# Kernel optimization log

Measured on AMD Instinct MI355X. Metric: run time of the kernel, lower is better.

## Reference

```python
import jax, jax.numpy as jnp
import numpy as np

N = 512
D = 512
# static upper-triangle pair indices (i < j)
_II, _JJ = np.triu_indices(N, k=1)
_II = jnp.asarray(_II)
_JJ = jnp.asarray(_JJ)


def setup_inputs() -> dict:
    key = jax.random.key(0)
    ks = jax.random.split(key, 9)
    s = 0.02
    return {
        'features': jax.random.normal(ks[0], (N, D), dtype=jnp.float32),
        # relation_classifier: Linear(2D->D), Linear(D->10)
        'cw1': jax.random.normal(ks[1], (2 * D, D), dtype=jnp.float32) * s,
        'cb1': jnp.zeros((D,), dtype=jnp.float32),
        'cw2': jax.random.normal(ks[2], (D, 10), dtype=jnp.float32) * s,
        'cb2': jnp.zeros((10,), dtype=jnp.float32),
        # relation_strength_calc: Linear(2D->D//2), Linear(D//2->1)
        'sw1': jax.random.normal(ks[3], (2 * D, D // 2), dtype=jnp.float32) * s,
        'sb1': jnp.zeros((D // 2,), dtype=jnp.float32),
        'sw2': jax.random.normal(ks[4], (D // 2, 1), dtype=jnp.float32) * s,
        'sb2': jnp.zeros((1,), dtype=jnp.float32),
    }


def reference(features, cw1, cb1, cw2, cb2, sw1, sb1, sw2, sb2):
    # cat([f_i, f_j]) @ W == f_i @ W[:D] + f_j @ W[D:]  (linear-split trick)
    # precompute per-node projections once, then gather per pair
    c_a = features @ cw1[:D]   # [N, D]
    c_b = features @ cw1[D:]   # [N, D]
    s_a = features @ sw1[:D]   # [N, D//2]
    s_b = features @ sw1[D:]   # [N, D//2]

    # classifier path
    h = jax.nn.relu(c_a[_II] + c_b[_JJ] + cb1)          # [P, D]
    relation_types = jax.nn.log_softmax(h @ cw2 + cb2)   # [P, 10]
    most_likely_relations = jnp.argmax(relation_types, axis=-1)  # [P]

    # strength path
    hs = jax.nn.relu(s_a[_II] + s_b[_JJ] + sb1)          # [P, D//2]
    relation_strengths = jax.nn.sigmoid(hs @ sw2 + sb2)   # [P, 1]

    return relation_types, most_likely_relations, relation_strengths
```

## Files before the change

kernel.cpp:

```cpp
#include <hip/hip_runtime.h>
#include <math.h>

#define NN 512
#define DD 512
#define NPAIRS 130816
#define TYPES_OFF 0
#define ARGMAX_OFF 1308160
#define STRENGTH_OFF 1438976

#define GAP_THRESH 2.5e-4f


__device__ __forceinline__ void fma64_step(
    const float4& a0, const float4& a1,
    const float4& b0, const float4& b1, const float4& b2, const float4& b3,
    double acc[2][4])
{
    const float av[2][4] = {{a0.x,a0.y,a0.z,a0.w},{a1.x,a1.y,a1.z,a1.w}};
    const float bv[4][4] = {{b0.x,b0.y,b0.z,b0.w},{b1.x,b1.y,b1.z,b1.w},
                            {b2.x,b2.y,b2.z,b2.w},{b3.x,b3.y,b3.z,b3.w}};
    #pragma unroll
    for (int kk = 0; kk < 4; ++kk) {
        double ad0 = (double)av[0][kk], ad1 = (double)av[1][kk];
        #pragma unroll
        for (int c = 0; c < 4; ++c) {
            double bd = (double)bv[kk][c];
            acc[0][c] = fma(ad0, bd, acc[0][c]);
            acc[1][c] = fma(ad1, bd, acc[1][c]);
        }
    }
}

__device__ __forceinline__ void fma32_step(
    const float4& a0, const float4& a1,
    const float4& b0, const float4& b1, const float4& b2, const float4& b3,
    float acc[2][4])
{
    const float av[2][4] = {{a0.x,a0.y,a0.z,a0.w},{a1.x,a1.y,a1.z,a1.w}};
    const float bv[4][4] = {{b0.x,b0.y,b0.z,b0.w},{b1.x,b1.y,b1.z,b1.w},
                            {b2.x,b2.y,b2.z,b2.w},{b3.x,b3.y,b3.z,b3.w}};
    #pragma unroll
    for (int kk = 0; kk < 4; ++kk) {
        #pragma unroll
        for (int c = 0; c < 4; ++c) {
            acc[0][c] = fmaf(av[0][kk], bv[kk][c], acc[0][c]);
            acc[1][c] = fmaf(av[1][kk], bv[kk][c], acc[1][c]);
        }
    }
}

__global__ __launch_bounds__(256, 4) void proj_kernel(
    const float* __restrict__ F, const float* __restrict__ cw1,
    const float* __restrict__ sw1,
    const float* __restrict__ cb1, const float* __restrict__ sb1,
    double* __restrict__ ca0, double* __restrict__ ca1,
    double* __restrict__ cb0, double* __restrict__ cbp1,
    float* __restrict__ sa0, float* __restrict__ sa1,
    float* __restrict__ sb0, float* __restrict__ sbp1)
{
    const int t = threadIdx.x;
    const int wid  = blockIdx.x * 4 + (t >> 6);
    const int lane = t & 63;
    const int mg = lane >> 4;
    const int nq = lane & 15;

    if (wid < 2048) {
        const int z  = wid & 1;
        const int r  = wid >> 1;
        const int nt = r & 15;
        const int mt = r >> 4;
        const int m0 = mt * 8;
        const int n  = nt * 64;
        const float* W = (n < 512) ? cw1 : cw1 + 512 * 512;
        const int n0   = (n < 512) ? n : n - 512;
        double* outp   = (n < 512) ? (z ? ca1 : ca0) : (z ? cbp1 : cb0);
        const bool addbias = (z == 0) && (n < 512);

        const int row0 = m0 + mg * 2;
        const int col0 = n0 + nq * 4;
        const float* pa0 = F + row0 * 512 + z * 256;
        const float* pa1 = pa0 + 512;
        const float* pb  = W + (z * 256) * 512 + col0;

        double acc[2][4];
        #pragma unroll
        for (int rr = 0; rr < 2; ++rr)
            #pragma unroll
            for (int cc = 0; cc < 4; ++cc) acc[rr][cc] = 0.0;

        float4 a0 = *(const float4*)(pa0);
        float4 a1 = *(const float4*)(pa1);
        float4 b0 = *(const float4*)(pb);
        float4 b1 = *(const float4*)(pb + 512);
        float4 b2 = *(const float4*)(pb + 1024);
        float4 b3 = *(const float4*)(pb + 1536);
        for (int s = 0; s < 63; ++s) {
            float4 na0 = *(const float4*)(pa0 + (s + 1) * 4);
            float4 na1 = *(const float4*)(pa1 + (s + 1) * 4);
            const float* nb = pb + (s + 1) * 2048;
            float4 nb0 = *(const float4*)(nb);
            float4 nb1 = *(const float4*)(nb + 512);
            float4 nb2 = *(const float4*)(nb + 1024);
            float4 nb3 = *(const float4*)(nb + 1536);
            fma64_step(a0, a1, b0, b1, b2, b3, acc);
            a0 = na0; a1 = na1; b0 = nb0; b1 = nb1; b2 = nb2; b3 = nb3;
        }
        fma64_step(a0, a1, b0, b1, b2, b3, acc);

        #pragma unroll
        for (int rr = 0; rr < 2; ++rr) {
            double v[4];
            #pragma unroll
            for (int cc = 0; cc < 4; ++cc) {
                v[cc] = acc[rr][cc];
                if (addbias) v[cc] += (double)cb1[col0 + cc];
            }
            double* dst = outp + (row0 + rr) * 512 + col0;
            *(double2*)(dst + 0) = make_double2(v[0], v[1]);
            *(double2*)(dst + 2) = make_double2(v[2], v[3]);
        }
    } else {
        const int w2 = wid - 2048;
        const int z  = w2 & 1;
        const int r  = w2 >> 1;
        const int nt = r & 7;
        const int mt = r >> 3;
        const int m0 = mt * 8;
        const int n  = nt * 64;
        const float* W = (n < 256) ? sw1 : sw1 + 512 * 256;
        const int n0   = (n < 256) ? n : n - 256;
        float* outp    = (n < 256) ? (z ? sa1 : sa0) : (z ? sbp1 : sb0);
        const bool addbias = (z == 0) && (n < 256);

        const int row0 = m0 + mg * 2;
        const int col0 = n0 + nq * 4;
        const float* pa0 = F + row0 * 512 + z * 256;
        const float* pa1 = pa0 + 512;
        const float* pb  = W + (z * 256) * 256 + col0;

        float acc[2][4];
        #pragma unroll
        for (int rr = 0; rr < 2; ++rr)
            #pragma unroll
            for (int cc = 0; cc < 4; ++cc) acc[rr][cc] = 0.f;

        float4 a0 = *(const float4*)(pa0);
        float4 a1 = *(const float4*)(pa1);
        float4 b0 = *(const float4*)(pb);
        float4 b1 = *(const float4*)(pb + 256);
        float4 b2 = *(const float4*)(pb + 512);
        float4 b3 = *(const float4*)(pb + 768);
        for (int s = 0; s < 63; ++s) {
            float4 na0 = *(const float4*)(pa0 + (s + 1) * 4);
            float4 na1 = *(const float4*)(pa1 + (s + 1) * 4);
            const float* nb = pb + (s + 1) * 1024;
            float4 nb0 = *(const float4*)(nb);
            float4 nb1 = *(const float4*)(nb + 256);
            float4 nb2 = *(const float4*)(nb + 512);
            float4 nb3 = *(const float4*)(nb + 768);
            fma32_step(a0, a1, b0, b1, b2, b3, acc);
            a0 = na0; a1 = na1; b0 = nb0; b1 = nb1; b2 = nb2; b3 = nb3;
        }
        fma32_step(a0, a1, b0, b1, b2, b3, acc);

        #pragma unroll
        for (int rr = 0; rr < 2; ++rr) {
            float4 v = make_float4(acc[rr][0], acc[rr][1], acc[rr][2], acc[rr][3]);
            if (addbias) {
                v.x += sb1[col0 + 0]; v.y += sb1[col0 + 1];
                v.z += sb1[col0 + 2]; v.w += sb1[col0 + 3];
            }
            *(float4*)(outp + (row0 + rr) * 256 + col0) = v;
        }
    }
}

__global__ __launch_bounds__(256, 4) void pair_kernel(
    const double* __restrict__ ca0, const double* __restrict__ ca1,
    const double* __restrict__ cb0, const double* __restrict__ cbp1,
    const float* __restrict__ sa0, const float* __restrict__ sa1,
    const float* __restrict__ sb0, const float* __restrict__ sbp1,
    const float* __restrict__ cw2, const float* __restrict__ cb2,
    const float* __restrict__ sw2, const float* __restrict__ sb2,
    float* __restrict__ out)
{
    const int b = blockIdx.x;
    int bi = (int)floorf((129.0f - sqrtf(16641.0f - 8.0f * (float)b)) * 0.5f);
    while ((bi + 1) * (129 - (bi + 1)) / 2 <= b) ++bi;
    while (bi * (129 - bi) / 2 > b) --bi;
    const int bj = bi + (b - bi * (129 - bi) / 2);
    const int i0 = bi * 8, j0 = bj * 8;

    const int t = threadIdx.x;
    const int q  = t >> 6;
    const int qu = __builtin_amdgcn_readfirstlane(q);
    const int l = t & 63;
    const int pi = l >> 3, pj = l & 7;
    const int i = i0 + pi, j = j0 + pj;

    __shared__ __align__(16) float smem[4352];
    float* sSa = smem;
    float* sSb = smem + 2176;
    float* sA  = smem;
    float* sB  = smem + 2176;
    float* lgbuf = smem;
    float* stbuf = smem + 1920;

    #pragma unroll
    for (int u = 0; u < 4; ++u) {
        int idx = u * 256 + t;
        int kq  = idx & 15;
        int row = (idx >> 4) & 7;
        int qq  = (idx >> 7) & 3;
        int arr = idx >> 9;
        int off = (arr ? (j0 + row) : (i0 + row)) * 256 + qq * 64 + kq * 4;
        const float* s0 = arr ? sb0 : sa0;
        const float* s1 = arr ? sbp1 : sa1;
        float4 v0 = *(const float4*)(s0 + off);
        float4 v1 = *(const float4*)(s1 + off);
        float4 v = make_float4(v0.x + v1.x, v0.y + v1.y, v0.z + v1.z, v0.w + v1.w);
        float* dst = (arr ? sSb : sSa) + (qq * 8 + row) * 68 + kq * 4;
        *(float4*)dst = v;
    }
    __syncthreads();
    float accs = 0.f;
    {
        const float* sw2q = sw2 + qu * 64;
        const float* ra = sSa + (q * 8 + pi) * 68;
        const float* rb = sSb + (q * 8 + pj) * 68;
        #pragma unroll 16
        for (int kk = 0; kk < 64; ++kk) {
            float h = fmaxf(ra[kk] + rb[kk], 0.f);
            accs = fmaf(h, sw2q[kk], accs);
        }
    }

    float lg[10];
    #pragma unroll
    for (int c = 0; c < 10; ++c) lg[c] = 0.f;

    for (int rnd = 0; rnd < 2; ++rnd) {
        __syncthreads();
        #pragma unroll
        for (int u = 0; u < 4; ++u) {
            int idx = u * 256 + t;
            int kq  = idx & 15;
            int row = (idx >> 4) & 7;
            int qq  = (idx >> 7) & 3;
            int arr = idx >> 9;
            int off = (arr ? (j0 + row) : (i0 + row)) * 512 + qq * 128 + rnd * 64 + kq * 4;
            const double* d0 = arr ? cb0 : ca0;
            const double* d1 = arr ? cbp1 : ca1;
            double2 x0 = *(const double2*)(d0 + off);
            double2 x1 = *(const double2*)(d0 + off + 2);
            double2 y0 = *(const double2*)(d1 + off);
            double2 y1 = *(const double2*)(d1 + off + 2);
            float4 v = make_float4((float)(x0.x + y0.x), (float)(x0.y + y0.y),
                                   (float)(x1.x + y1.x), (float)(x1.y + y1.y));
            float* dst = (arr ? sB : sA) + (qq * 8 + row) * 68 + kq * 4;
            *(float4*)dst = v;
        }
        __syncthreads();
        const float* ra = sA + (q * 8 + pi) * 68;
        const float* rb = sB + (q * 8 + pj) * 68;
        const float* wr = cw2 + (qu * 128 + rnd * 64) * 10;
        #pragma unroll 8
        for (int kk = 0; kk < 64; ++kk) {
            float h = fmaxf(ra[kk] + rb[kk], 0.f);
            const float* w = wr + kk * 10;
            #pragma unroll
            for (int c = 0; c < 10; ++c) lg[c] = fmaf(h, w[c], lg[c]);
        }
    }

    __syncthreads();
    if (q > 0) {
        float* dst = lgbuf + ((q - 1) * 64 + l) * 10;
        #pragma unroll
        for (int c = 0; c < 10; ++c) dst[c] = lg[c];
        stbuf[(q - 1) * 64 + l] = accs;
    }
    __syncthreads();
    if (q == 0) {
        #pragma unroll
        for (int w = 0; w < 3; ++w) {
            const float* srcb = lgbuf + (w * 64 + l) * 10;
            #pragma unroll
            for (int c = 0; c < 10; ++c) lg[c] += srcb[c];
        }
        float st = accs + stbuf[l] + stbuf[64 + l] + stbuf[128 + l] + sb2[0];

        #pragma unroll
        for (int c = 0; c < 10; ++c) lg[c] += cb2[c];

        float mx = lg[0], mx2 = -3.0e38f; int am2 = 0;
        #pragma unroll
        for (int c = 1; c < 10; ++c) {
            if (lg[c] > mx) { mx2 = mx; mx = lg[c]; am2 = c; }
            else if (lg[c] > mx2) mx2 = lg[c];
        }

        unsigned long long m = __ballot((j > i) && (mx - mx2 < GAP_THRESH));
        while (m) {
            const int s = __ffsll((unsigned long long)m) - 1; m &= (m - 1);
            const int si = i0 + (s >> 3), sj = j0 + (s & 7);
            double part[10];
            #pragma unroll
            for (int c = 0; c < 10; ++c) part[c] = 0.0;
            const int kb = l * 8;
            #pragma unroll 2
            for (int kk = 0; kk < 8; ++kk) {
                const int k = kb + kk;
                double h = fmax(ca0[si * 512 + k] + ca1[si * 512 + k]
                              + cb0[sj * 512 + k] + cbp1[sj * 512 + k], 0.0);
                const float* w = cw2 + k * 10;
                #pragma unroll
                for (int c = 0; c < 10; ++c) part[c] = fma(h, (double)w[c], part[c]);
            }
            #pragma unroll
            for (int off = 32; off > 0; off >>= 1) {
                #pragma unroll
                for (int c = 0; c < 10; ++c) part[c] += __shfl_xor(part[c], off, 64);
            }
            double bmx = part[0] + (double)cb2[0]; int ba = 0;
            #pragma unroll
            for (int c = 1; c < 10; ++c) {
                double v = part[c] + (double)cb2[c];
                if (v > bmx) { bmx = v; ba = c; }
            }
            if (l == s) am2 = ba;
        }

        float tf[10]; float ssum = 0.f;
        #pragma unroll
        for (int c = 0; c < 10; ++c) { tf[c] = lg[c] - mx; ssum += __expf(tf[c]); }
        float ls = __logf(ssum);

        if (j > i) {
            const int p = i * 511 - (i * (i - 1)) / 2 + (j - i - 1);
            float* tp = out + TYPES_OFF + p * 10;
            #pragma unroll
            for (int c = 0; c < 10; ++c) tp[c] = tf[c] - ls;
            out[ARGMAX_OFF + p] = (float)am2;
            out[STRENGTH_OFF + p] = 1.0f / (1.0f + __expf(-st));
        }
    }
}

extern "C" void kernel_launch(void* const* d_in, const int* in_sizes, int n_in,
                              void* d_out, int out_size, void* d_ws, size_t ws_size,
                              hipStream_t stream) {
    const float* F   = (const float*)d_in[0];
    const float* cw1 = (const float*)d_in[1];
    const float* cb1 = (const float*)d_in[2];
    const float* cw2 = (const float*)d_in[3];
    const float* cb2 = (const float*)d_in[4];
    const float* sw1 = (const float*)d_in[5];
    const float* sb1 = (const float*)d_in[6];
    const float* sw2 = (const float*)d_in[7];
    const float* sb2 = (const float*)d_in[8];
    float* out = (float*)d_out;

    char* ws = (char*)d_ws;
    double* ca0  = (double*)(ws);
    double* ca1  = (double*)(ws + 2097152);
    double* cb0  = (double*)(ws + 4194304);
    double* cbp1 = (double*)(ws + 6291456);
    float*  sa0  = (float*)(ws + 8388608);
    float*  sa1  = (float*)(ws + 8912896);
    float*  sb0  = (float*)(ws + 9437184);
    float*  sbp1 = (float*)(ws + 9961472);

    hipLaunchKernelGGL(proj_kernel, dim3(768), dim3(256), 0, stream,
                       F, cw1, sw1, cb1, sb1,
                       ca0, ca1, cb0, cbp1, sa0, sa1, sb0, sbp1);
    hipLaunchKernelGGL(pair_kernel, dim3(2080), dim3(256), 0, stream,
                       ca0, ca1, cb0, cbp1, sa0, sa1, sb0, sbp1,
                       cw2, cb2, sw2, sb2, out);
}
```

Measured before the change: 146.1 us.

## Halve per-thread FP64 projection tile and use packed FP32 FMAs in pair kernel

```diff
diff --git a/kernel.cpp b/kernel.cpp
--- a/kernel.cpp
+++ b/kernel.cpp
@@ -11,23 +11,46 @@
 #define GAP_THRESH 2.5e-4f
 
 
-__device__ __forceinline__ void fma64_step(
+typedef float f32x2 __attribute__((ext_vector_type(2)));
+
+__device__ __forceinline__ f32x2 pk_add(f32x2 a, f32x2 b) {
+    f32x2 d;
+    asm("v_pk_add_f32 %0, %1, %2" : "=v"(d) : "v"(a), "v"(b));
+    return d;
+}
+__device__ __forceinline__ f32x2 pk_fma(f32x2 a, f32x2 b, f32x2 c) {
+    f32x2 d;
+    asm("v_pk_fma_f32 %0, %1, %2, %3" : "=v"(d) : "v"(a), "s"(b), "v"(c));
+    return d;
+}
+__device__ __forceinline__ f32x2 pk_fma_lo(f32x2 a, f32x2 b, f32x2 c) {
+    f32x2 d;
+    asm("v_pk_fma_f32 %0, %1, %2, %3 op_sel:[0,0,0] op_sel_hi:[0,1,1]"
+        : "=v"(d) : "v"(a), "s"(b), "v"(c));
+    return d;
+}
+__device__ __forceinline__ f32x2 pk_fma_hi(f32x2 a, f32x2 b, f32x2 c) {
+    f32x2 d;
+    asm("v_pk_fma_f32 %0, %1, %2, %3 op_sel:[1,0,0] op_sel_hi:[1,1,1]"
+        : "=v"(d) : "v"(a), "s"(b), "v"(c));
+    return d;
+}
+
+__device__ __forceinline__ void fma64_step2(
     const float4& a0, const float4& a1,
-    const float4& b0, const float4& b1, const float4& b2, const float4& b3,
-    double acc[2][4])
+    const float2& b0, const float2& b1, const float2& b2, const float2& b3,
+    double acc[2][2])
 {
     const float av[2][4] = {{a0.x,a0.y,a0.z,a0.w},{a1.x,a1.y,a1.z,a1.w}};
-    const float bv[4][4] = {{b0.x,b0.y,b0.z,b0.w},{b1.x,b1.y,b1.z,b1.w},
-                            {b2.x,b2.y,b2.z,b2.w},{b3.x,b3.y,b3.z,b3.w}};
+    const float bv[4][2] = {{b0.x,b0.y},{b1.x,b1.y},{b2.x,b2.y},{b3.x,b3.y}};
     #pragma unroll
     for (int kk = 0; kk < 4; ++kk) {
         double ad0 = (double)av[0][kk], ad1 = (double)av[1][kk];
-        #pragma unroll
-        for (int c = 0; c < 4; ++c) {
-            double bd = (double)bv[kk][c];
-            acc[0][c] = fma(ad0, bd, acc[0][c]);
-            acc[1][c] = fma(ad1, bd, acc[1][c]);
-        }
+        double bd0 = (double)bv[kk][0], bd1 = (double)bv[kk][1];
+        acc[0][0] = fma(ad0, bd0, acc[0][0]);
+        acc[0][1] = fma(ad0, bd1, acc[0][1]);
+        acc[1][0] = fma(ad1, bd0, acc[1][0]);
+        acc[1][1] = fma(ad1, bd1, acc[1][1]);
     }
 }
 
@@ -64,63 +87,57 @@
     const int mg = lane >> 4;
     const int nq = lane & 15;
 
-    if (wid < 2048) {
+    if (wid < 4096) {
         const int z  = wid & 1;
         const int r  = wid >> 1;
-        const int nt = r & 15;
-        const int mt = r >> 4;
+        const int nt = r & 31;
+        const int mt = r >> 5;
         const int m0 = mt * 8;
-        const int n  = nt * 64;
+        const int n  = nt * 32;
         const float* W = (n < 512) ? cw1 : cw1 + 512 * 512;
         const int n0   = (n < 512) ? n : n - 512;
         double* outp   = (n < 512) ? (z ? ca1 : ca0) : (z ? cbp1 : cb0);
         const bool addbias = (z == 0) && (n < 512);
 
         const int row0 = m0 + mg * 2;
-        const int col0 = n0 + nq * 4;
+        const int col0 = n0 + nq * 2;
         const float* pa0 = F + row0 * 512 + z * 256;
         const float* pa1 = pa0 + 512;
         const float* pb  = W + (z * 256) * 512 + col0;
 
-        double acc[2][4];
-        #pragma unroll
-        for (int rr = 0; rr < 2; ++rr)
-            #pragma unroll
-            for (int cc = 0; cc < 4; ++cc) acc[rr][cc] = 0.0;
+        double acc[2][2];
+        acc[0][0] = acc[0][1] = acc[1][0] = acc[1][1] = 0.0;
 
         float4 a0 = *(const float4*)(pa0);
         float4 a1 = *(const float4*)(pa1);
-        float4 b0 = *(const float4*)(pb);
-        float4 b1 = *(const float4*)(pb + 512);
-        float4 b2 = *(const float4*)(pb + 1024);
-        float4 b3 = *(const float4*)(pb + 1536);
+        float2 b0 = *(const float2*)(pb);
+        float2 b1 = *(const float2*)(pb + 512);
+        float2 b2 = *(const float2*)(pb + 1024);
+        float2 b3 = *(const float2*)(pb + 1536);
         for (int s = 0; s < 63; ++s) {
             float4 na0 = *(const float4*)(pa0 + (s + 1) * 4);
             float4 na1 = *(const float4*)(pa1 + (s + 1) * 4);
             const float* nb = pb + (s + 1) * 2048;
-            float4 nb0 = *(const float4*)(nb);
-            float4 nb1 = *(const float4*)(nb + 512);
-            float4 nb2 = *(const float4*)(nb + 1024);
-            float4 nb3 = *(const float4*)(nb + 1536);
-            fma64_step(a0, a1, b0, b1, b2, b3, acc);
+            float2 nb0 = *(const float2*)(nb);
+            float2 nb1 = *(const float2*)(nb + 512);
+            float2 nb2 = *(const float2*)(nb + 1024);
+            float2 nb3 = *(const float2*)(nb + 1536);
+            fma64_step2(a0, a1, b0, b1, b2, b3, acc);
             a0 = na0; a1 = na1; b0 = nb0; b1 = nb1; b2 = nb2; b3 = nb3;
         }
-        fma64_step(a0, a1, b0, b1, b2, b3, acc);
+        fma64_step2(a0, a1, b0, b1, b2, b3, acc);
 
         #pragma unroll
         for (int rr = 0; rr < 2; ++rr) {
-            double v[4];
-            #pragma unroll
-            for (int cc = 0; cc < 4; ++cc) {
-                v[cc] = acc[rr][cc];
-                if (addbias) v[cc] += (double)cb1[col0 + cc];
-            }
-            double* dst = outp + (row0 + rr) * 512 + col0;
-            *(double2*)(dst + 0) = make_double2(v[0], v[1]);
-            *(double2*)(dst + 2) = make_double2(v[2], v[3]);
+            double v0 = acc[rr][0], v1 = acc[rr][1];
+            if (addbias) {
+                v0 += (double)cb1[col0 + 0];
+                v1 += (double)cb1[col0 + 1];
+            }
+            *(double2*)(outp + (row0 + rr) * 512 + col0) = make_double2(v0, v1);
         }
     } else {
-        const int w2 = wid - 2048;
+        const int w2 = wid - 4096;
         const int z  = w2 & 1;
         const int r  = w2 >> 1;
         const int nt = r & 7;
@@ -228,16 +245,24 @@
         const float* sw2q = sw2 + qu * 64;
         const float* ra = sSa + (q * 8 + pi) * 68;
         const float* rb = sSb + (q * 8 + pj) * 68;
-        #pragma unroll 16
-        for (int kk = 0; kk < 64; ++kk) {
-            float h = fmaxf(ra[kk] + rb[kk], 0.f);
-            accs = fmaf(h, sw2q[kk], accs);
-        }
-    }
-
-    float lg[10];
+        f32x2 acc2 = {0.f, 0.f};
+        #pragma unroll 8
+        for (int kk = 0; kk < 64; kk += 2) {
+            f32x2 a2 = *(const f32x2*)(ra + kk);
+            f32x2 b2 = *(const f32x2*)(rb + kk);
+            f32x2 s2 = pk_add(a2, b2);
+            f32x2 h2;
+            h2.x = fmaxf(s2.x, 0.f);
+            h2.y = fmaxf(s2.y, 0.f);
+            f32x2 w2p = *(const f32x2*)(sw2q + kk);
+            acc2 = pk_fma(h2, w2p, acc2);
+        }
+        accs = acc2.x + acc2.y;
+    }
+
+    f32x2 acc5[5];
     #pragma unroll
-    for (int c = 0; c < 10; ++c) lg[c] = 0.f;
+    for (int cc = 0; cc < 5; ++cc) acc5[cc] = (f32x2){0.f, 0.f};
 
     for (int rnd = 0; rnd < 2; ++rnd) {
         __syncthreads();
@@ -264,14 +289,28 @@
         const float* ra = sA + (q * 8 + pi) * 68;
         const float* rb = sB + (q * 8 + pj) * 68;
         const float* wr = cw2 + (qu * 128 + rnd * 64) * 10;
-        #pragma unroll 8
-        for (int kk = 0; kk < 64; ++kk) {
-            float h = fmaxf(ra[kk] + rb[kk], 0.f);
-            const float* w = wr + kk * 10;
-            #pragma unroll
-            for (int c = 0; c < 10; ++c) lg[c] = fmaf(h, w[c], lg[c]);
-        }
-    }
+        #pragma unroll 2
+        for (int kk = 0; kk < 64; kk += 2) {
+            f32x2 ra2 = *(const f32x2*)(ra + kk);
+            f32x2 rb2 = *(const f32x2*)(rb + kk);
+            f32x2 s2 = pk_add(ra2, rb2);
+            f32x2 h2;
+            h2.x = fmaxf(s2.x, 0.f);
+            h2.y = fmaxf(s2.y, 0.f);
+            const float* w0 = wr + kk * 10;
+            #pragma unroll
+            for (int cc = 0; cc < 5; ++cc) {
+                f32x2 wk0 = *(const f32x2*)(w0 + 2 * cc);
+                f32x2 wk1 = *(const f32x2*)(w0 + 10 + 2 * cc);
+                acc5[cc] = pk_fma_lo(h2, wk0, acc5[cc]);
+                acc5[cc] = pk_fma_hi(h2, wk1, acc5[cc]);
+            }
+        }
+    }
+
+    float lg[10];
+    #pragma unroll
+    for (int cc = 0; cc < 5; ++cc) { lg[2*cc] = acc5[cc].x; lg[2*cc+1] = acc5[cc].y; }
 
     __syncthreads();
     if (q > 0) {
@@ -371,7 +410,7 @@
     float*  sb0  = (float*)(ws + 9437184);
     float*  sbp1 = (float*)(ws + 9961472);
 
-    hipLaunchKernelGGL(proj_kernel, dim3(768), dim3(256), 0, stream,
+    hipLaunchKernelGGL(proj_kernel, dim3(1280), dim3(256), 0, stream,
                        F, cw1, sw1, cb1, sb1,
                        ca0, ca1, cb0, cbp1, sa0, sa1, sb0, sbp1);
     hipLaunchKernelGGL(pair_kernel, dim3(2080), dim3(256), 0, stream,
```

Result: slower. 200.4 us (+37.2%).

## Stage projection weights in shared memory and vectorize pair-kernel LDS reads

Applied to the files above, without the earlier changes.

```diff
diff --git a/kernel.cpp b/kernel.cpp
--- a/kernel.cpp
+++ b/kernel.cpp
@@ -10,26 +10,6 @@
 
 #define GAP_THRESH 2.5e-4f
 
-
-__device__ __forceinline__ void fma64_step(
-    const float4& a0, const float4& a1,
-    const float4& b0, const float4& b1, const float4& b2, const float4& b3,
-    double acc[2][4])
-{
-    const float av[2][4] = {{a0.x,a0.y,a0.z,a0.w},{a1.x,a1.y,a1.z,a1.w}};
-    const float bv[4][4] = {{b0.x,b0.y,b0.z,b0.w},{b1.x,b1.y,b1.z,b1.w},
-                            {b2.x,b2.y,b2.z,b2.w},{b3.x,b3.y,b3.z,b3.w}};
-    #pragma unroll
-    for (int kk = 0; kk < 4; ++kk) {
-        double ad0 = (double)av[0][kk], ad1 = (double)av[1][kk];
-        #pragma unroll
-        for (int c = 0; c < 4; ++c) {
-            double bd = (double)bv[kk][c];
-            acc[0][c] = fma(ad0, bd, acc[0][c]);
-            acc[1][c] = fma(ad1, bd, acc[1][c]);
-        }
-    }
-}
 
 __device__ __forceinline__ void fma32_step(
     const float4& a0, const float4& a1,
@@ -58,54 +38,81 @@
     float* __restrict__ sa0, float* __restrict__ sa1,
     float* __restrict__ sb0, float* __restrict__ sbp1)
 {
+    __shared__ __align__(16) float sW[2][16][68];
+
     const int t = threadIdx.x;
-    const int wid  = blockIdx.x * 4 + (t >> 6);
     const int lane = t & 63;
     const int mg = lane >> 4;
     const int nq = lane & 15;
 
-    if (wid < 2048) {
-        const int z  = wid & 1;
-        const int r  = wid >> 1;
-        const int nt = r & 15;
-        const int mt = r >> 4;
-        const int m0 = mt * 8;
+    if (blockIdx.x < 512) {
+        const int b  = blockIdx.x;
+        const int z  = b & 1;
+        const int nt = (b >> 1) & 15;
+        const int mt = b >> 5;
+        const int w  = t >> 6;
         const int n  = nt * 64;
         const float* W = (n < 512) ? cw1 : cw1 + 512 * 512;
         const int n0   = (n < 512) ? n : n - 512;
         double* outp   = (n < 512) ? (z ? ca1 : ca0) : (z ? cbp1 : cb0);
         const bool addbias = (z == 0) && (n < 512);
 
-        const int row0 = m0 + mg * 2;
+        const int row0 = mt * 32 + w * 8 + mg * 2;
         const int col0 = n0 + nq * 4;
+
+        const int cg = t & 15, kr = t >> 4;
+        const float* wsrc = W + (z * 256 + kr) * 512 + n0 + cg * 4;
+
+        {
+            float4 w0 = *(const float4*)(wsrc);
+            *(float4*)&sW[0][kr][cg * 4] = w0;
+        }
+        __syncthreads();
+
+        double acc[2][4];
+        #pragma unroll
+        for (int rr = 0; rr < 2; ++rr)
+            #pragma unroll
+            for (int cc = 0; cc < 4; ++cc) acc[rr][cc] = 0.0;
+
         const float* pa0 = F + row0 * 512 + z * 256;
         const float* pa1 = pa0 + 512;
-        const float* pb  = W + (z * 256) * 512 + col0;
-
-        double acc[2][4];
-        #pragma unroll
-        for (int rr = 0; rr < 2; ++rr)
-            #pragma unroll
-            for (int cc = 0; cc < 4; ++cc) acc[rr][cc] = 0.0;
-
         float4 a0 = *(const float4*)(pa0);
         float4 a1 = *(const float4*)(pa1);
-        float4 b0 = *(const float4*)(pb);
-        float4 b1 = *(const float4*)(pb + 512);
-        float4 b2 = *(const float4*)(pb + 1024);
-        float4 b3 = *(const float4*)(pb + 1536);
-        for (int s = 0; s < 63; ++s) {
-            float4 na0 = *(const float4*)(pa0 + (s + 1) * 4);
-            float4 na1 = *(const float4*)(pa1 + (s + 1) * 4);
-            const float* nb = pb + (s + 1) * 2048;
-            float4 nb0 = *(const float4*)(nb);
-            float4 nb1 = *(const float4*)(nb + 512);
-            float4 nb2 = *(const float4*)(nb + 1024);
-            float4 nb3 = *(const float4*)(nb + 1536);
-            fma64_step(a0, a1, b0, b1, b2, b3, acc);
-            a0 = na0; a1 = na1; b0 = nb0; b1 = nb1; b2 = nb2; b3 = nb3;
-        }
-        fma64_step(a0, a1, b0, b1, b2, b3, acc);
+
+        for (int r = 0; r < 16; ++r) {
+            float4 wnext;
+            if (r < 15) wnext = *(const float4*)(wsrc + (r + 1) * 8192);
+            const int buf = r & 1;
+            #pragma unroll
+            for (int s4 = 0; s4 < 4; ++s4) {
+                const int kb  = r * 16 + s4 * 4;
+                const int kbn = (kb < 252) ? kb + 4 : 252;
+                float4 na0 = *(const float4*)(pa0 + kbn);
+                float4 na1 = *(const float4*)(pa1 + kbn);
+                const float av0[4] = {a0.x, a0.y, a0.z, a0.w};
+                const float av1[4] = {a1.x, a1.y, a1.z, a1.w};
+                #pragma unroll
+                for (int kk = 0; kk < 4; ++kk) {
+                    float4 bq = *(const float4*)&sW[buf][s4 * 4 + kk][nq * 4];
+                    double ad0 = (double)av0[kk], ad1 = (double)av1[kk];
+                    double bd0 = (double)bq.x, bd1 = (double)bq.y;
+                    double bd2 = (double)bq.z, bd3 = (double)bq.w;
+                    acc[0][0] = fma(ad0, bd0, acc[0][0]);
+                    acc[0][1] = fma(ad0, bd1, acc[0][1]);
+                    acc[0][2] = fma(ad0, bd2, acc[0][2]);
+                    acc[0][3] = fma(ad0, bd3, acc[0][3]);
+                    acc[1][0] = fma(ad1, bd0, acc[1][0]);
+                    acc[1][1] = fma(ad1, bd1, acc[1][1]);
+                    acc[1][2] = fma(ad1, bd2, acc[1][2]);
+                    acc[1][3] = fma(ad1, bd3, acc[1][3]);
+                }
+                a0 = na0; a1 = na1;
+            }
+            __syncthreads();
+            if (r < 15) *(float4*)&sW[(r + 1) & 1][kr][cg * 4] = wnext;
+            __syncthreads();
+        }
 
         #pragma unroll
         for (int rr = 0; rr < 2; ++rr) {
@@ -120,7 +127,7 @@
             *(double2*)(dst + 2) = make_double2(v[2], v[3]);
         }
     } else {
-        const int w2 = wid - 2048;
+        const int w2 = (blockIdx.x - 512) * 4 + (t >> 6);
         const int z  = w2 & 1;
         const int r  = w2 >> 1;
         const int nt = r & 7;
@@ -175,7 +182,7 @@
     }
 }
 
-__global__ __launch_bounds__(256, 4) void pair_kernel(
+__global__ __launch_bounds__(256, 6) void pair_kernel(
     const double* __restrict__ ca0, const double* __restrict__ ca1,
     const double* __restrict__ cb0, const double* __restrict__ cbp1,
     const float* __restrict__ sa0, const float* __restrict__ sa1,
@@ -228,11 +235,16 @@
         const float* sw2q = sw2 + qu * 64;
         const float* ra = sSa + (q * 8 + pi) * 68;
         const float* rb = sSb + (q * 8 + pj) * 68;
-        #pragma unroll 16
-        for (int kk = 0; kk < 64; ++kk) {
-            float h = fmaxf(ra[kk] + rb[kk], 0.f);
-            accs = fmaf(h, sw2q[kk], accs);
-        }
+        float p0 = 0.f, p1 = 0.f, p2 = 0.f, p3 = 0.f;
+        for (int kk = 0; kk < 64; kk += 4) {
+            float4 a4 = *(const float4*)(ra + kk);
+            float4 b4 = *(const float4*)(rb + kk);
+            p0 = fmaf(fmaxf(a4.x + b4.x, 0.f), sw2q[kk + 0], p0);
+            p1 = fmaf(fmaxf(a4.y + b4.y, 0.f), sw2q[kk + 1], p1);
+            p2 = fmaf(fmaxf(a4.z + b4.z, 0.f), sw2q[kk + 2], p2);
+            p3 = fmaf(fmaxf(a4.w + b4.w, 0.f), sw2q[kk + 3], p3);
+        }
+        accs = (p0 + p1) + (p2 + p3);
     }
 
     float lg[10];
@@ -264,12 +276,22 @@
         const float* ra = sA + (q * 8 + pi) * 68;
         const float* rb = sB + (q * 8 + pj) * 68;
         const float* wr = cw2 + (qu * 128 + rnd * 64) * 10;
-        #pragma unroll 8
-        for (int kk = 0; kk < 64; ++kk) {
-            float h = fmaxf(ra[kk] + rb[kk], 0.f);
+        for (int kk = 0; kk < 64; kk += 4) {
+            float4 ra4 = *(const float4*)(ra + kk);
+            float4 rb4 = *(const float4*)(rb + kk);
+            float h0 = fmaxf(ra4.x + rb4.x, 0.f);
+            float h1 = fmaxf(ra4.y + rb4.y, 0.f);
+            float h2 = fmaxf(ra4.z + rb4.z, 0.f);
+            float h3 = fmaxf(ra4.w + rb4.w, 0.f);
             const float* w = wr + kk * 10;
             #pragma unroll
-            for (int c = 0; c < 10; ++c) lg[c] = fmaf(h, w[c], lg[c]);
+            for (int c = 0; c < 10; ++c) lg[c] = fmaf(h0, w[c], lg[c]);
+            #pragma unroll
+            for (int c = 0; c < 10; ++c) lg[c] = fmaf(h1, w[10 + c], lg[c]);
+            #pragma unroll
+            for (int c = 0; c < 10; ++c) lg[c] = fmaf(h2, w[20 + c], lg[c]);
+            #pragma unroll
+            for (int c = 0; c < 10; ++c) lg[c] = fmaf(h3, w[30 + c], lg[c]);
         }
     }
 
```

Measured after the change: 201.2 us. +37.7%, slower.

## Precombine split double projections into float arrays before pair kernel

Applied to the files above, without the earlier changes.

```diff
diff --git a/kernel.cpp b/kernel.cpp
--- a/kernel.cpp
+++ b/kernel.cpp
@@ -175,11 +175,41 @@
     }
 }
 
-__global__ __launch_bounds__(256, 4) void pair_kernel(
+__global__ __launch_bounds__(256) void combine_kernel(
     const double* __restrict__ ca0, const double* __restrict__ ca1,
     const double* __restrict__ cb0, const double* __restrict__ cbp1,
     const float* __restrict__ sa0, const float* __restrict__ sa1,
     const float* __restrict__ sb0, const float* __restrict__ sbp1,
+    float* __restrict__ cfa, float* __restrict__ cfb,
+    float* __restrict__ sfa, float* __restrict__ sfb)
+{
+    const int t = blockIdx.x * 256 + threadIdx.x;
+    {
+        const int e = 2 * t;
+        double2 x = *(const double2*)(ca0 + e);
+        double2 y = *(const double2*)(ca1 + e);
+        *(float2*)(cfa + e) = make_float2((float)(x.x + y.x), (float)(x.y + y.y));
+        double2 u = *(const double2*)(cb0 + e);
+        double2 v = *(const double2*)(cbp1 + e);
+        *(float2*)(cfb + e) = make_float2((float)(u.x + v.x), (float)(u.y + v.y));
+    }
+    if (t < 65536) {
+        const bool second = t >= 32768;
+        const int e = (second ? (t - 32768) : t) * 4;
+        const float* s0 = second ? sb0 : sa0;
+        const float* s1 = second ? sbp1 : sa1;
+        float* dst      = second ? sfb : sfa;
+        float4 a = *(const float4*)(s0 + e);
+        float4 b = *(const float4*)(s1 + e);
+        *(float4*)(dst + e) = make_float4(a.x + b.x, a.y + b.y, a.z + b.z, a.w + b.w);
+    }
+}
+
+__global__ __launch_bounds__(256, 4) void pair_kernel(
+    const double* __restrict__ ca0, const double* __restrict__ ca1,
+    const double* __restrict__ cb0, const double* __restrict__ cbp1,
+    const float* __restrict__ cfa, const float* __restrict__ cfb,
+    const float* __restrict__ sfa, const float* __restrict__ sfb,
     const float* __restrict__ cw2, const float* __restrict__ cb2,
     const float* __restrict__ sw2, const float* __restrict__ sb2,
     float* __restrict__ out)
@@ -214,11 +244,8 @@
         int qq  = (idx >> 7) & 3;
         int arr = idx >> 9;
         int off = (arr ? (j0 + row) : (i0 + row)) * 256 + qq * 64 + kq * 4;
-        const float* s0 = arr ? sb0 : sa0;
-        const float* s1 = arr ? sbp1 : sa1;
-        float4 v0 = *(const float4*)(s0 + off);
-        float4 v1 = *(const float4*)(s1 + off);
-        float4 v = make_float4(v0.x + v1.x, v0.y + v1.y, v0.z + v1.z, v0.w + v1.w);
+        const float* src = arr ? sfb : sfa;
+        float4 v = *(const float4*)(src + off);
         float* dst = (arr ? sSb : sSa) + (qq * 8 + row) * 68 + kq * 4;
         *(float4*)dst = v;
     }
@@ -228,11 +255,16 @@
         const float* sw2q = sw2 + qu * 64;
         const float* ra = sSa + (q * 8 + pi) * 68;
         const float* rb = sSb + (q * 8 + pj) * 68;
-        #pragma unroll 16
-        for (int kk = 0; kk < 64; ++kk) {
-            float h = fmaxf(ra[kk] + rb[kk], 0.f);
-            accs = fmaf(h, sw2q[kk], accs);
-        }
+        float p0 = 0.f, p1 = 0.f, p2 = 0.f, p3 = 0.f;
+        for (int kk = 0; kk < 64; kk += 4) {
+            float4 a4 = *(const float4*)(ra + kk);
+            float4 b4 = *(const float4*)(rb + kk);
+            p0 = fmaf(fmaxf(a4.x + b4.x, 0.f), sw2q[kk + 0], p0);
+            p1 = fmaf(fmaxf(a4.y + b4.y, 0.f), sw2q[kk + 1], p1);
+            p2 = fmaf(fmaxf(a4.z + b4.z, 0.f), sw2q[kk + 2], p2);
+            p3 = fmaf(fmaxf(a4.w + b4.w, 0.f), sw2q[kk + 3], p3);
+        }
+        accs = (p0 + p1) + (p2 + p3);
     }
 
     float lg[10];
@@ -249,14 +281,8 @@
             int qq  = (idx >> 7) & 3;
             int arr = idx >> 9;
             int off = (arr ? (j0 + row) : (i0 + row)) * 512 + qq * 128 + rnd * 64 + kq * 4;
-            const double* d0 = arr ? cb0 : ca0;
-            const double* d1 = arr ? cbp1 : ca1;
-            double2 x0 = *(const double2*)(d0 + off);
-            double2 x1 = *(const double2*)(d0 + off + 2);
-            double2 y0 = *(const double2*)(d1 + off);
-            double2 y1 = *(const double2*)(d1 + off + 2);
-            float4 v = make_float4((float)(x0.x + y0.x), (float)(x0.y + y0.y),
-                                   (float)(x1.x + y1.x), (float)(x1.y + y1.y));
+            const float* src = arr ? cfb : cfa;
+            float4 v = *(const float4*)(src + off);
             float* dst = (arr ? sB : sA) + (qq * 8 + row) * 68 + kq * 4;
             *(float4*)dst = v;
         }
@@ -264,12 +290,22 @@
         const float* ra = sA + (q * 8 + pi) * 68;
         const float* rb = sB + (q * 8 + pj) * 68;
         const float* wr = cw2 + (qu * 128 + rnd * 64) * 10;
-        #pragma unroll 8
-        for (int kk = 0; kk < 64; ++kk) {
-            float h = fmaxf(ra[kk] + rb[kk], 0.f);
+        for (int kk = 0; kk < 64; kk += 4) {
+            float4 ra4 = *(const float4*)(ra + kk);
+            float4 rb4 = *(const float4*)(rb + kk);
+            float h0 = fmaxf(ra4.x + rb4.x, 0.f);
+            float h1 = fmaxf(ra4.y + rb4.y, 0.f);
+            float h2 = fmaxf(ra4.z + rb4.z, 0.f);
+            float h3 = fmaxf(ra4.w + rb4.w, 0.f);
             const float* w = wr + kk * 10;
             #pragma unroll
-            for (int c = 0; c < 10; ++c) lg[c] = fmaf(h, w[c], lg[c]);
+            for (int c = 0; c < 10; ++c) lg[c] = fmaf(h0, w[c], lg[c]);
+            #pragma unroll
+            for (int c = 0; c < 10; ++c) lg[c] = fmaf(h1, w[10 + c], lg[c]);
+            #pragma unroll
+            for (int c = 0; c < 10; ++c) lg[c] = fmaf(h2, w[20 + c], lg[c]);
+            #pragma unroll
+            for (int c = 0; c < 10; ++c) lg[c] = fmaf(h3, w[30 + c], lg[c]);
         }
     }
 
@@ -370,11 +406,18 @@
     float*  sa1  = (float*)(ws + 8912896);
     float*  sb0  = (float*)(ws + 9437184);
     float*  sbp1 = (float*)(ws + 9961472);
+    float*  cfa  = (float*)(ws + 10485760);
+    float*  cfb  = (float*)(ws + 11534336);
+    float*  sfa  = (float*)(ws + 12582912);
+    float*  sfb  = (float*)(ws + 13107200);
 
     hipLaunchKernelGGL(proj_kernel, dim3(768), dim3(256), 0, stream,
                        F, cw1, sw1, cb1, sb1,
                        ca0, ca1, cb0, cbp1, sa0, sa1, sb0, sbp1);
+    hipLaunchKernelGGL(combine_kernel, dim3(512), dim3(256), 0, stream,
+                       ca0, ca1, cb0, cbp1, sa0, sa1, sb0, sbp1,
+                       cfa, cfb, sfa, sfb);
     hipLaunchKernelGGL(pair_kernel, dim3(2080), dim3(256), 0, stream,
-                       ca0, ca1, cb0, cbp1, sa0, sa1, sb0, sbp1,
+                       ca0, ca1, cb0, cbp1, cfa, cfb, sfa, sfb,
                        cw2, cb2, sw2, sb2, out);
 }
```

New measurement: 147.2 us. Within noise of the previous version (+0.7%).
